# Performance work log

Hardware: AMD Instinct MI355X
Metric: run time of the kernel (lower is better)

## Reference

```python
import jax, jax.numpy as jnp
import numpy as np

BS, T, N, DIM = 16, 2048, 2048, 128

def setup_inputs() -> dict:
    key = jax.random.key(0)
    k1, k2, k3 = jax.random.split(key, 3)
    aud_feats = jax.random.normal(k1, (BS, T, DIM), dtype=jnp.float32)
    semantic_feats = jax.random.normal(k2, (BS, N, DIM), dtype=jnp.float32)
    W = jax.random.normal(k3, (1, 3 * DIM), dtype=jnp.float32) * 0.02
    b = jnp.zeros((1,), dtype=jnp.float32)
    return {"aud_feats": aud_feats, "semantic_feats": semantic_feats, "W": W, "b": b}


def reference(aud_feats, semantic_feats, W, b):
    # S[b,i,j] = Linear(cat(h_t, h_n, h_t*h_n)) decomposed into three rank-1 pieces
    dim = aud_feats.shape[-1]
    w1 = W[0, :dim]
    w2 = W[0, dim:2 * dim]
    w3 = W[0, 2 * dim:]
    S = (jnp.einsum('btd,d->bt', aud_feats, w1)[:, :, None]
         + jnp.einsum('bnd,d->bn', semantic_feats, w2)[:, None, :]
         + jnp.einsum('btd,bnd->btn', aud_feats * w3, semantic_feats)
         + b[0])  # [bs, t, n]
    at = jax.nn.softmax(S, axis=2)                     # attend over semantic tokens
    bw = jax.nn.softmax(jnp.max(S, axis=2), axis=1)    # [bs, t]
    h_con_a2 = jnp.einsum('bt,btd->bd', bw, aud_feats)[:, None, :]   # [bs,1,d], broadcasts
    h_con_w = jnp.einsum('btn,bnd->btd', at, semantic_feats)          # [bs,t,d]
    flow_matrix = jnp.concatenate(
        [aud_feats, h_con_w, aud_feats * h_con_w, aud_feats * h_con_a2], axis=2)
    return flow_matrix
```

## Files before the change

kernel.cpp:

```cpp
#include <hip/hip_runtime.h>
#include <stdint.h>

#define BSZ 16
#define TT  2048
#define NSEM 2048
#define DIM 128
#define ORS 1024
#define PSTR 68

typedef __attribute__((ext_vector_type(8))) short short8;
typedef __attribute__((ext_vector_type(4))) float floatx4;

__device__ __forceinline__ unsigned short f2bf(float f){
  unsigned u = __float_as_uint(f);
  return (unsigned short)((u + 0x7fffu + ((u >> 16) & 1u)) >> 16);
}
__device__ __forceinline__ void ld8f(const float* p, float* v){
  floatx4 a = *(const floatx4*)p;
  floatx4 b = *(const floatx4*)(p + 4);
  v[0]=a[0]; v[1]=a[1]; v[2]=a[2]; v[3]=a[3];
  v[4]=b[0]; v[5]=b[1]; v[6]=b[2]; v[7]=b[3];
}
__device__ __forceinline__ void gload_lds16(const unsigned short* g, unsigned short* l){
  __builtin_amdgcn_global_load_lds((const __attribute__((address_space(1))) void*)g,
                                   (__attribute__((address_space(3))) void*)l, 16, 0, 0);
}


__global__ __launch_bounds__(256) void prep_kernel(const float* __restrict__ sem,
                                                   const float* __restrict__ W,
                                                   float* __restrict__ colB,
                                                   unsigned short* __restrict__ outw){
  __shared__ unsigned short tile[DIM * 72];
  const int tid = threadIdx.x;
  const int b  = blockIdx.x >> 5;
  const int n0 = (blockIdx.x & 31) * 64;

  const int r = tid >> 2, cc = tid & 3, c = cc * 32;
  const float* src = sem + ((size_t)(b * NSEM + n0 + r)) * DIM + c;
  float v[32];
  ld8f(src, v); ld8f(src + 8, v + 8); ld8f(src + 16, v + 16); ld8f(src + 24, v + 24);
  alignas(16) unsigned short bf[32];
  float cpart = 0.f;
  #pragma unroll
  for (int j = 0; j < 32; ++j){
    bf[j] = f2bf(v[j]);
    cpart += v[j] * W[DIM + c + j];
  }
  {
    const int nblk = (n0 >> 4) + (r >> 4);
    const int l15r = r & 15;
    unsigned short* base = outw + ((size_t)(b * TT + nblk * 4 + cc)) * ORS + 512;
    const uint4* s4 = (const uint4*)bf;
    #pragma unroll
    for (int q = 0; q < 4; ++q)
      *(uint4*)(base + q * 128 + l15r * 8) = s4[q];
  }
  #pragma unroll
  for (int j = 0; j < 32; ++j) tile[(c + j) * 72 + r] = bf[j];
  cpart += __shfl_xor(cpart, 1);
  cpart += __shfl_xor(cpart, 2);
  if (cc == 0) colB[b * NSEM + n0 + r] = cpart;
  __syncthreads();

  {
    const int kt = tid >> 7, dc = (tid >> 4) & 7, l15 = tid & 15;
    const int d = dc * 16 + l15;
    const int ntile = n0 >> 6;
    unsigned short* base = outw + ((size_t)(b * TT + 512 + ntile * 16 + kt * 8 + dc)) * ORS + 512;
    #pragma unroll
    for (int q = 0; q < 4; ++q){
      uint4 tv = *(const uint4*)&tile[d * 72 + kt * 32 + q * 8];
      *(uint4*)(base + q * 128 + l15 * 8) = tv;
    }
  }
}

__global__ __launch_bounds__(256, 2) void flash_kernel(const float* __restrict__ aud,
                                                    const float* __restrict__ W,
                                                    const float* __restrict__ colB,
                                                    float* __restrict__ m_ws,
                                                    float* __restrict__ outf,
                                                    const unsigned short* __restrict__ outw){
  __shared__ alignas(16) unsigned short kvt[2][16][512];
  __shared__ alignas(16) unsigned short pbuf[4][16 * PSTR];

  const int tid  = threadIdx.x;
  const int wv   = tid >> 6;
  const int lane = tid & 63;
  const int quad = lane >> 4;
  const int l15  = lane & 15;
  const int b    = blockIdx.x >> 5;
  const int t0w  = (blockIdx.x & 31) * 64 + wv * 16;

  const unsigned short* stage = outw + (size_t)b * TT * ORS + 512 + lane * 8;

  #pragma unroll
  for (int jj = 0; jj < 4; ++jj){
    const int j = wv * 4 + jj;
    gload_lds16(stage + (size_t)j * ORS, &kvt[0][j][0]);
  }

  const float* audRow = aud + ((size_t)b * TT + t0w + l15) * DIM;
  short8 qf[4];
  float rowA_part = 0.f;
  #pragma unroll
  for (int kc = 0; kc < 4; ++kc){
    int d0 = kc * 32 + quad * 8;
    float av[8], w3v[8], w1v[8];
    ld8f(audRow + d0, av);
    ld8f(W + 2 * DIM + d0, w3v);
    ld8f(W + d0, w1v);
    alignas(16) unsigned short tmp[8];
    #pragma unroll
    for (int j = 0; j < 8; ++j){
      tmp[j] = f2bf(av[j] * w3v[j]);
      rowA_part += av[j] * w1v[j];
    }
    qf[kc] = *(const short8*)tmp;
  }
  rowA_part += __shfl_xor(rowA_part, 16);
  rowA_part += __shfl_xor(rowA_part, 32);

  float m_run = -1e30f, l_run = 0.f;
  float m_true = -1e30f;
  floatx4 o[8];
  #pragma unroll
  for (int dc = 0; dc < 8; ++dc){
    #pragma unroll
    for (int r = 0; r < 4; ++r) o[dc][r] = 0.f;
  }

  const float* colBb = colB + b * NSEM;
  unsigned short* pb = &pbuf[wv][0];

  __syncthreads();

  for (int it = 0; it < 32; ++it){
    const int n0 = it * 64;

    const int cV = 512 + it * 16;
    short8 vf[16];
    #pragma unroll
    for (int i = 0; i < 16; ++i) vf[i] = *(const short8*)(stage + (size_t)(cV + i) * ORS);

    if (it + 1 < 32){
      #pragma unroll
      for (int jj = 0; jj < 4; ++jj){
        const int j = wv * 4 + jj;
        gload_lds16(stage + (size_t)((it + 1) * 16 + j) * ORS, &kvt[(it + 1) & 1][j][0]);
      }
    }
    __builtin_amdgcn_sched_barrier(0);

    const unsigned short* kvb = &kvt[it & 1][0][0] + lane * 8;

    floatx4 cbv[4];
    #pragma unroll
    for (int s = 0; s < 4; ++s) cbv[s] = *(const floatx4*)(colBb + n0 + s*16 + quad*4);

    floatx4 sacc[4];
    #pragma unroll
    for (int s = 0; s < 4; ++s){ sacc[s][0]=0.f; sacc[s][1]=0.f; sacc[s][2]=0.f; sacc[s][3]=0.f; }
    #pragma unroll
    for (int s = 0; s < 4; ++s){
      #pragma unroll
      for (int kc = 0; kc < 4; ++kc){
        short8 kf = *(const short8*)(kvb + (s*4 + kc) * 512);
        sacc[s] = __builtin_amdgcn_mfma_f32_16x16x32_bf16(kf, qf[kc], sacc[s], 0, 0, 0);
      }
    }

    float v[4][4];
    #pragma unroll
    for (int s = 0; s < 4; ++s){
      #pragma unroll
      for (int r = 0; r < 4; ++r) v[s][r] = sacc[s][r] + cbv[s][r];
    }
    float mq[4];
    #pragma unroll
    for (int s = 0; s < 4; ++s)
      mq[s] = fmaxf(fmaxf(v[s][0], v[s][1]), fmaxf(v[s][2], v[s][3]));
    float mx = fmaxf(fmaxf(mq[0], mq[1]), fmaxf(mq[2], mq[3]));
    mx = fmaxf(mx, __shfl_xor(mx, 16));
    mx = fmaxf(mx, __shfl_xor(mx, 32));
    m_true = fmaxf(m_true, mx);

    const bool defer = (__all(mx - m_run <= 8.0f) != 0);
    float al = 1.0f;
    if (!defer){
      float mnew = fmaxf(m_run, mx);
      al = __expf(m_run - mnew);
      m_run = mnew;
    }
    float e[4][4];
    #pragma unroll
    for (int s = 0; s < 4; ++s){
      #pragma unroll
      for (int r = 0; r < 4; ++r) e[s][r] = __expf(v[s][r] - m_run);
    }
    float sq[4];
    #pragma unroll
    for (int s = 0; s < 4; ++s)
      sq[s] = (e[s][0] + e[s][1]) + (e[s][2] + e[s][3]);
    float ps = (sq[0] + sq[1]) + (sq[2] + sq[3]);
    ps += __shfl_xor(ps, 16);
    ps += __shfl_xor(ps, 32);
    l_run = l_run * al + ps;

    #pragma unroll
    for (int s = 0; s < 4; ++s){
      unsigned u0 = (unsigned)f2bf(e[s][0]) | ((unsigned)f2bf(e[s][1]) << 16);
      unsigned u1 = (unsigned)f2bf(e[s][2]) | ((unsigned)f2bf(e[s][3]) << 16);
      unsigned short* pr = pb + l15 * PSTR + s * 16 + quad * 4;
      *(unsigned*)(pr)     = u0;
      *(unsigned*)(pr + 2) = u1;
    }

    if (!defer){
      float aB[4];
      #pragma unroll
      for (int r = 0; r < 4; ++r) aB[r] = __shfl(al, quad*4 + r);
      #pragma unroll
      for (int dc = 0; dc < 8; ++dc){
        #pragma unroll
        for (int r = 0; r < 4; ++r) o[dc][r] *= aB[r];
      }
    }

    asm volatile("s_waitcnt lgkmcnt(0)" ::: "memory");
    short8 pf0 = *(const short8*)(pb + l15 * PSTR + quad * 8);
    short8 pf1 = *(const short8*)(pb + l15 * PSTR + 32 + quad * 8);

    #pragma unroll
    for (int kt = 0; kt < 2; ++kt){
      short8 pf = kt ? pf1 : pf0;
      #pragma unroll
      for (int dc = 0; dc < 8; ++dc)
        o[dc] = __builtin_amdgcn_mfma_f32_16x16x32_bf16(pf, vf[kt*8 + dc], o[dc], 0, 0, 0);
    }

    __syncthreads();
  }

  float rl = 1.0f / l_run;
  float rB[4];
  #pragma unroll
  for (int r = 0; r < 4; ++r) rB[r] = __shfl(rl, quad*4 + r);
  float* outB = outf + ((size_t)b * TT + t0w) * 512 + 128;
  #pragma unroll
  for (int dc = 0; dc < 8; ++dc){
    #pragma unroll
    for (int r = 0; r < 4; ++r)
      outB[(size_t)(quad*4 + r) * 512 + dc*16 + l15] = o[dc][r] * rB[r];
  }
  if (quad == 0)
    m_ws[(size_t)b * TT + t0w + l15] = m_true + rowA_part;
}

__global__ __launch_bounds__(256) void bw1_kernel(const float* __restrict__ m_ws,
                                                  float* __restrict__ pmax){
  __shared__ float sA[4];
  const int b = blockIdx.x >> 3, ch = blockIdx.x & 7, tid = threadIdx.x;
  float v = m_ws[(size_t)b * TT + ch * 256 + tid];
  #pragma unroll
  for (int off = 1; off < 64; off <<= 1) v = fmaxf(v, __shfl_xor(v, off));
  if ((tid & 63) == 0) sA[tid >> 6] = v;
  __syncthreads();
  if (tid == 0)
    pmax[blockIdx.x] = fmaxf(fmaxf(sA[0], sA[1]), fmaxf(sA[2], sA[3]));
}

__global__ __launch_bounds__(256) void bw2_kernel(const float* __restrict__ aud,
                                                  const float* __restrict__ m_ws,
                                                  const float* __restrict__ pmax,
                                                  float* __restrict__ gpart,
                                                  float* __restrict__ part){
  __shared__ float wbuf[256];
  __shared__ float red[16 * 128];
  __shared__ float gs4[4];
  const int b = blockIdx.x >> 3, ch = blockIdx.x & 7, tid = threadIdx.x;

  float gmax = pmax[b * 8];
  #pragma unroll
  for (int i = 1; i < 8; ++i) gmax = fmaxf(gmax, pmax[b * 8 + i]);

  float w = __expf(m_ws[(size_t)b * TT + ch * 256 + tid] - gmax);
  wbuf[tid] = w;
  float sm = w;
  #pragma unroll
  for (int off = 1; off < 64; off <<= 1) sm += __shfl_xor(sm, off);
  if ((tid & 63) == 0) gs4[tid >> 6] = sm;
  __syncthreads();
  if (tid == 0) gpart[blockIdx.x] = (gs4[0] + gs4[1]) + (gs4[2] + gs4[3]);

  const int dg = tid & 15, q = tid >> 4;
  float acc[8] = {0,0,0,0,0,0,0,0};
  const float* ab = aud + ((size_t)b * TT + ch * 256 + q * 16) * DIM + dg * 8;
  for (int i = 0; i < 16; ++i){
    float av[8];
    ld8f(ab + (size_t)i * DIM, av);
    float wt = wbuf[q * 16 + i];
    #pragma unroll
    for (int j = 0; j < 8; ++j) acc[j] += wt * av[j];
  }
  #pragma unroll
  for (int j = 0; j < 8; ++j) red[q * 128 + dg * 8 + j] = acc[j];
  __syncthreads();
  if (tid < 128){
    float s = 0.f;
    #pragma unroll
    for (int q2 = 0; q2 < 16; ++q2) s += red[q2 * 128 + tid];
    part[(size_t)blockIdx.x * 128 + tid] = s;
  }
}

__global__ __launch_bounds__(256) void epi_kernel(const float* __restrict__ aud,
                                                  const float* __restrict__ gpart,
                                                  const float* __restrict__ part,
                                                  float* __restrict__ out){
  __shared__ float a2s[DIM];
  int id = blockIdx.x * 256 + threadIdx.x;
  int c = id & 15;
  int t = (id >> 4) & (TT - 1);
  int b = id >> 15;
  size_t row = (size_t)b * TT + t;

  if (threadIdx.x < 128){
    const int d = threadIdx.x;
    float s = 0.f, g = 0.f;
    #pragma unroll
    for (int ch = 0; ch < 8; ++ch){
      s += part[(size_t)(b * 8 + ch) * 128 + d];
      g += gpart[b * 8 + ch];
    }
    a2s[d] = s / g;
  }
  __syncthreads();

  float av[8], gv[8], hv[8];
  ld8f(aud + row * DIM + c * 8, av);
  ld8f(out + row * 512 + 128 + c * 8, hv);
  #pragma unroll
  for (int j = 0; j < 8; ++j) gv[j] = a2s[c * 8 + j];

  floatx4 o0a, o0b, o2a, o2b, o3a, o3b;
  #pragma unroll
  for (int j = 0; j < 4; ++j){
    o0a[j] = av[j];           o0b[j] = av[4+j];
    o2a[j] = av[j]*hv[j];     o2b[j] = av[4+j]*hv[4+j];
    o3a[j] = av[j]*gv[j];     o3b[j] = av[4+j]*gv[4+j];
  }
  float* ob = out + row * 512 + c * 8;
  *(floatx4*)(ob)       = o0a;  *(floatx4*)(ob + 4)   = o0b;
  *(floatx4*)(ob + 256) = o2a;  *(floatx4*)(ob + 260) = o2b;
  *(floatx4*)(ob + 384) = o3a;  *(floatx4*)(ob + 388) = o3b;
}

extern "C" void kernel_launch(void* const* d_in, const int* in_sizes, int n_in,
                              void* d_out, int out_size, void* d_ws, size_t ws_size,
                              hipStream_t stream){
  const float* aud = (const float*)d_in[0];
  const float* sem = (const float*)d_in[1];
  const float* W   = (const float*)d_in[2];
  float* out = (float*)d_out;
  unsigned short* outw = (unsigned short*)d_out;

  float* ws    = (float*)d_ws;
  float* m_ws  = ws;
  float* colB  = m_ws + (size_t)BSZ * TT;
  float* a2_ws = colB + (size_t)BSZ * NSEM;
  float* pmax  = a2_ws + BSZ * DIM;
  float* gpart = pmax + 128;
  float* part  = gpart + 128;

  prep_kernel <<<512, 256, 0, stream>>>(sem, W, colB, outw);
  flash_kernel<<<512, 256, 0, stream>>>(aud, W, colB, m_ws, out, outw);
  bw1_kernel  <<<128, 256, 0, stream>>>(m_ws, pmax);
  bw2_kernel  <<<128, 256, 0, stream>>>(aud, m_ws, pmax, gpart, part);
  epi_kernel  <<<(BSZ * TT * 16) / 256, 256, 0, stream>>>(aud, gpart, part, out);
}
```

Before: 197.3 us.

## Split flash kernel over two KV halves per block with in-LDS merge, exp2 softmax

The flash kernel now runs 512 threads per block. Two wave groups each process half of the semantic tokens and keep separate online-softmax state, which is merged through LDS at the end. This doubles in-flight waves and halves the serial loop length per wave. Softmax switches to the base-2 domain: log2e is folded into q and colB, exp2 is used, and the final max is rescaled by ln2. The P buffer uses XOR swizzling with packed bf16 conversion to reduce LDS bank conflicts and conversion instructions. In exchange the kernel pays extra LDS use, a merge step and register pressure under launch_bounds(512,4).

Result: slower. 372.6 us (+88.9%).

```diff
diff --git a/kernel.cpp b/kernel.cpp
--- a/kernel.cpp
+++ b/kernel.cpp
@@ -6,7 +6,8 @@
 #define NSEM 2048
 #define DIM 128
 #define ORS 1024
-#define PSTR 68
+#define LOG2E 1.4426950408889634f
+#define LN2   0.6931471805599453f
 
 typedef __attribute__((ext_vector_type(8))) short short8;
 typedef __attribute__((ext_vector_type(4))) float floatx4;
@@ -14,6 +15,18 @@
 __device__ __forceinline__ unsigned short f2bf(float f){
   unsigned u = __float_as_uint(f);
   return (unsigned short)((u + 0x7fffu + ((u >> 16) & 1u)) >> 16);
+}
+__device__ __forceinline__ unsigned pkbf(float a, float b){
+  unsigned r;
+  asm("v_cvt_pk_bf16_f32 %0, %1, %2" : "=v"(r) : "v"(a), "v"(b));
+  return r;
+}
+__device__ __forceinline__ float e2(float x){
+#if __has_builtin(__builtin_amdgcn_exp2f)
+  return __builtin_amdgcn_exp2f(x);
+#else
+  return exp2f(x);
+#endif
 }
 __device__ __forceinline__ void ld8f(const float* p, float* v){
   floatx4 a = *(const floatx4*)p;
@@ -60,7 +73,7 @@
   for (int j = 0; j < 32; ++j) tile[(c + j) * 72 + r] = bf[j];
   cpart += __shfl_xor(cpart, 1);
   cpart += __shfl_xor(cpart, 2);
-  if (cc == 0) colB[b * NSEM + n0 + r] = cpart;
+  if (cc == 0) colB[b * NSEM + n0 + r] = cpart * LOG2E;
   __syncthreads();
 
   {
@@ -76,30 +89,30 @@
   }
 }
 
-__global__ __launch_bounds__(256, 2) void flash_kernel(const float* __restrict__ aud,
+__global__ __launch_bounds__(512, 4) void flash_kernel(const float* __restrict__ aud,
                                                     const float* __restrict__ W,
                                                     const float* __restrict__ colB,
                                                     float* __restrict__ m_ws,
                                                     float* __restrict__ outf,
                                                     const unsigned short* __restrict__ outw){
-  __shared__ alignas(16) unsigned short kvt[2][16][512];
-  __shared__ alignas(16) unsigned short pbuf[4][16 * PSTR];
+  __shared__ alignas(16) unsigned short kvt[2][2][16][512];
+  __shared__ alignas(16) unsigned short pbuf[8][1024];
 
   const int tid  = threadIdx.x;
   const int wv   = tid >> 6;
   const int lane = tid & 63;
   const int quad = lane >> 4;
   const int l15  = lane & 15;
+  const int h    = wv >> 2;
+  const int tg   = wv & 3;
   const int b    = blockIdx.x >> 5;
-  const int t0w  = (blockIdx.x & 31) * 64 + wv * 16;
+  const int t0w  = (blockIdx.x & 31) * 64 + tg * 16;
 
   const unsigned short* stage = outw + (size_t)b * TT * ORS + 512 + lane * 8;
 
   #pragma unroll
-  for (int jj = 0; jj < 4; ++jj){
-    const int j = wv * 4 + jj;
-    gload_lds16(stage + (size_t)j * ORS, &kvt[0][j][0]);
-  }
+  for (int jj = 0; jj < 4; ++jj)
+    gload_lds16(stage + (size_t)(h * 256 + tg * 4 + jj) * ORS, &kvt[h][0][tg * 4 + jj][0]);
 
   const float* audRow = aud + ((size_t)b * TT + t0w + l15) * DIM;
   short8 qf[4];
@@ -114,7 +127,7 @@
     alignas(16) unsigned short tmp[8];
     #pragma unroll
     for (int j = 0; j < 8; ++j){
-      tmp[j] = f2bf(av[j] * w3v[j]);
+      tmp[j] = f2bf(av[j] * (w3v[j] * LOG2E));
       rowA_part += av[j] * w1v[j];
     }
     qf[kc] = *(const short8*)tmp;
@@ -133,31 +146,31 @@
 
   const float* colBb = colB + b * NSEM;
   unsigned short* pb = &pbuf[wv][0];
-
-  __syncthreads();
-
-  for (int it = 0; it < 32; ++it){
-    const int n0 = it * 64;
-
-    const int cV = 512 + it * 16;
+  const int swz = (l15 & 7);
+
+  __syncthreads();
+
+  for (int it = 0; it < 16; ++it){
+    const int n0 = h * 1024 + it * 64;
+
+    floatx4 cbv[4];
+    #pragma unroll
+    for (int s = 0; s < 4; ++s) cbv[s] = *(const floatx4*)(colBb + n0 + s*16 + quad*4);
+
+    if (it + 1 < 16){
+      #pragma unroll
+      for (int jj = 0; jj < 4; ++jj)
+        gload_lds16(stage + (size_t)(h * 256 + (it + 1) * 16 + tg * 4 + jj) * ORS,
+                    &kvt[h][(it + 1) & 1][tg * 4 + jj][0]);
+    }
+
+    const int cV = 512 + (h * 16 + it) * 16;
     short8 vf[16];
     #pragma unroll
     for (int i = 0; i < 16; ++i) vf[i] = *(const short8*)(stage + (size_t)(cV + i) * ORS);
-
-    if (it + 1 < 32){
-      #pragma unroll
-      for (int jj = 0; jj < 4; ++jj){
-        const int j = wv * 4 + jj;
-        gload_lds16(stage + (size_t)((it + 1) * 16 + j) * ORS, &kvt[(it + 1) & 1][j][0]);
-      }
-    }
     __builtin_amdgcn_sched_barrier(0);
 
-    const unsigned short* kvb = &kvt[it & 1][0][0] + lane * 8;
-
-    floatx4 cbv[4];
-    #pragma unroll
-    for (int s = 0; s < 4; ++s) cbv[s] = *(const floatx4*)(colBb + n0 + s*16 + quad*4);
+    const unsigned short* kvb = &kvt[h][it & 1][0][0] + lane * 8;
 
     floatx4 sacc[4];
     #pragma unroll
@@ -190,14 +203,14 @@
     float al = 1.0f;
     if (!defer){
       float mnew = fmaxf(m_run, mx);
-      al = __expf(m_run - mnew);
+      al = e2(m_run - mnew);
       m_run = mnew;
     }
     float e[4][4];
     #pragma unroll
     for (int s = 0; s < 4; ++s){
       #pragma unroll
-      for (int r = 0; r < 4; ++r) e[s][r] = __expf(v[s][r] - m_run);
+      for (int r = 0; r < 4; ++r) e[s][r] = e2(v[s][r] - m_run);
     }
     float sq[4];
     #pragma unroll
@@ -210,11 +223,11 @@
 
     #pragma unroll
     for (int s = 0; s < 4; ++s){
-      unsigned u0 = (unsigned)f2bf(e[s][0]) | ((unsigned)f2bf(e[s][1]) << 16);
-      unsigned u1 = (unsigned)f2bf(e[s][2]) | ((unsigned)f2bf(e[s][3]) << 16);
-      unsigned short* pr = pb + l15 * PSTR + s * 16 + quad * 4;
-      *(unsigned*)(pr)     = u0;
-      *(unsigned*)(pr + 2) = u1;
+      unsigned u0 = pkbf(e[s][0], e[s][1]);
+      unsigned u1 = pkbf(e[s][2], e[s][3]);
+      const int chk = 2*s + (quad >> 1);
+      unsigned short* pr = pb + l15 * 64 + ((chk ^ swz) << 3) + (quad & 1) * 4;
+      *(uint64_t*)pr = (uint64_t)u0 | ((uint64_t)u1 << 32);
     }
 
     if (!defer){
@@ -229,8 +242,8 @@
     }
 
     asm volatile("s_waitcnt lgkmcnt(0)" ::: "memory");
-    short8 pf0 = *(const short8*)(pb + l15 * PSTR + quad * 8);
-    short8 pf1 = *(const short8*)(pb + l15 * PSTR + 32 + quad * 8);
+    short8 pf0 = *(const short8*)(pb + l15 * 64 + ((quad       ^ swz) << 3));
+    short8 pf1 = *(const short8*)(pb + l15 * 64 + (((4 | quad) ^ swz) << 3));
 
     #pragma unroll
     for (int kt = 0; kt < 2; ++kt){
@@ -243,19 +256,48 @@
     __syncthreads();
   }
 
-  float rl = 1.0f / l_run;
-  float rB[4];
-  #pragma unroll
-  for (int r = 0; r < 4; ++r) rB[r] = __shfl(rl, quad*4 + r);
-  float* outB = outf + ((size_t)b * TT + t0w) * 512 + 128;
-  #pragma unroll
-  for (int dc = 0; dc < 8; ++dc){
-    #pragma unroll
-    for (int r = 0; r < 4; ++r)
-      outB[(size_t)(quad*4 + r) * 512 + dc*16 + l15] = o[dc][r] * rB[r];
-  }
-  if (quad == 0)
-    m_ws[(size_t)b * TT + t0w + l15] = m_true + rowA_part;
+  float* Ob  = (float*)(&kvt[0][0][0][0]);
+  float* mlp = Ob + 4 * 16 * 128;
+  if (h == 1){
+    #pragma unroll
+    for (int dc = 0; dc < 8; ++dc){
+      #pragma unroll
+      for (int r = 0; r < 4; ++r)
+        Ob[(tg * 16 + quad * 4 + r) * 128 + dc * 16 + l15] = o[dc][r];
+    }
+    if (quad == 0){
+      mlp[tg * 48 +      l15] = m_run;
+      mlp[tg * 48 + 16 + l15] = l_run;
+      mlp[tg * 48 + 32 + l15] = m_true;
+    }
+  }
+  __syncthreads();
+  if (h == 0){
+    float mp  = mlp[tg * 48 +      l15];
+    float lp  = mlp[tg * 48 + 16 + l15];
+    float mtp = mlp[tg * 48 + 32 + l15];
+    float M  = fmaxf(m_run, mp);
+    float sA = e2(m_run - M);
+    float sB = e2(mp - M);
+    float lm = l_run * sA + lp * sB;
+    float mt = fmaxf(m_true, mtp);
+    float rl = 1.0f / lm;
+    float fa = sA * rl, fb = sB * rl;
+    float fA[4], fB[4];
+    #pragma unroll
+    for (int r = 0; r < 4; ++r){ fA[r] = __shfl(fa, quad*4 + r); fB[r] = __shfl(fb, quad*4 + r); }
+    float* outB = outf + ((size_t)b * TT + t0w) * 512 + 128;
+    #pragma unroll
+    for (int dc = 0; dc < 8; ++dc){
+      #pragma unroll
+      for (int r = 0; r < 4; ++r){
+        float op = Ob[(tg * 16 + quad * 4 + r) * 128 + dc * 16 + l15];
+        outB[(size_t)(quad*4 + r) * 512 + dc*16 + l15] = o[dc][r] * fA[r] + op * fB[r];
+      }
+    }
+    if (quad == 0)
+      m_ws[(size_t)b * TT + t0w + l15] = mt * LN2 + rowA_part;
+  }
 }
 
 __global__ __launch_bounds__(256) void bw1_kernel(const float* __restrict__ m_ws,
@@ -375,7 +417,7 @@
   float* part  = gpart + 128;
 
   prep_kernel <<<512, 256, 0, stream>>>(sem, W, colB, outw);
-  flash_kernel<<<512, 256, 0, stream>>>(aud, W, colB, m_ws, out, outw);
+  flash_kernel<<<512, 512, 0, stream>>>(aud, W, colB, m_ws, out, outw);
   bw1_kernel  <<<128, 256, 0, stream>>>(m_ws, pmax);
   bw2_kernel  <<<128, 256, 0, stream>>>(aud, m_ws, pmax, gpart, part);
   epi_kernel  <<<(BSZ * TT * 16) / 256, 256, 0, stream>>>(aud, gpart, part, out);
```

## Split attention over key halves with merge kernel and base-2 exponentials

Applied to the files above, without the earlier changes.

The flash kernel now splits the semantic-token dimension into two halves, doubling the block count to 1024. Each half writes unnormalized partial outputs and running max/sum statistics into spare regions of the output buffer, and a new merge kernel combines them with a log-sum-exp rescale. Scores are pre-scaled by log2(e) so the kernel can use exp2 in place of exp, and bf16 packing uses the hardware pack-convert instruction. The aim is more parallelism and occupancy on the GPU. The cost is an extra kernel launch and extra global traffic for the partial results.

Measured after the change: 215.0 us. 1.09x slower.

```diff
diff --git a/kernel.cpp b/kernel.cpp
--- a/kernel.cpp
+++ b/kernel.cpp
@@ -7,6 +7,8 @@
 #define DIM 128
 #define ORS 1024
 #define PSTR 68
+#define LOG2E 1.4426950408889634f
+#define LN2   0.6931471805599453f
 
 typedef __attribute__((ext_vector_type(8))) short short8;
 typedef __attribute__((ext_vector_type(4))) float floatx4;
@@ -14,6 +16,18 @@
 __device__ __forceinline__ unsigned short f2bf(float f){
   unsigned u = __float_as_uint(f);
   return (unsigned short)((u + 0x7fffu + ((u >> 16) & 1u)) >> 16);
+}
+__device__ __forceinline__ unsigned pkbf(float a, float b){
+  unsigned r;
+  asm("v_cvt_pk_bf16_f32 %0, %1, %2" : "=v"(r) : "v"(a), "v"(b));
+  return r;
+}
+__device__ __forceinline__ float e2(float x){
+#if __has_builtin(__builtin_amdgcn_exp2f)
+  return __builtin_amdgcn_exp2f(x);
+#else
+  return exp2f(x);
+#endif
 }
 __device__ __forceinline__ void ld8f(const float* p, float* v){
   floatx4 a = *(const floatx4*)p;
@@ -60,7 +74,7 @@
   for (int j = 0; j < 32; ++j) tile[(c + j) * 72 + r] = bf[j];
   cpart += __shfl_xor(cpart, 1);
   cpart += __shfl_xor(cpart, 2);
-  if (cc == 0) colB[b * NSEM + n0 + r] = cpart;
+  if (cc == 0) colB[b * NSEM + n0 + r] = cpart * LOG2E;
   __syncthreads();
 
   {
@@ -79,7 +93,6 @@
 __global__ __launch_bounds__(256, 2) void flash_kernel(const float* __restrict__ aud,
                                                     const float* __restrict__ W,
                                                     const float* __restrict__ colB,
-                                                    float* __restrict__ m_ws,
                                                     float* __restrict__ outf,
                                                     const unsigned short* __restrict__ outw){
   __shared__ alignas(16) unsigned short kvt[2][16][512];
@@ -90,15 +103,18 @@
   const int lane = tid & 63;
   const int quad = lane >> 4;
   const int l15  = lane & 15;
-  const int b    = blockIdx.x >> 5;
-  const int t0w  = (blockIdx.x & 31) * 64 + wv * 16;
+  const int b    = blockIdx.x >> 6;
+  const int sub  = blockIdx.x & 63;
+  const int tb   = sub >> 1;
+  const int h    = sub & 1;
+  const int t0w  = tb * 64 + wv * 16;
 
   const unsigned short* stage = outw + (size_t)b * TT * ORS + 512 + lane * 8;
 
   #pragma unroll
   for (int jj = 0; jj < 4; ++jj){
     const int j = wv * 4 + jj;
-    gload_lds16(stage + (size_t)j * ORS, &kvt[0][j][0]);
+    gload_lds16(stage + (size_t)(h * 256 + j) * ORS, &kvt[0][j][0]);
   }
 
   const float* audRow = aud + ((size_t)b * TT + t0w + l15) * DIM;
@@ -114,7 +130,7 @@
     alignas(16) unsigned short tmp[8];
     #pragma unroll
     for (int j = 0; j < 8; ++j){
-      tmp[j] = f2bf(av[j] * w3v[j]);
+      tmp[j] = f2bf(av[j] * (w3v[j] * LOG2E));
       rowA_part += av[j] * w1v[j];
     }
     qf[kc] = *(const short8*)tmp;
@@ -136,19 +152,21 @@
 
   __syncthreads();
 
-  for (int it = 0; it < 32; ++it){
-    const int n0 = it * 64;
-
-    const int cV = 512 + it * 16;
+  for (int it = 0; it < 16; ++it){
+    const int nt = h * 16 + it;
+    const int n0 = nt * 64;
+
+    const int cV = 512 + nt * 16;
     short8 vf[16];
     #pragma unroll
     for (int i = 0; i < 16; ++i) vf[i] = *(const short8*)(stage + (size_t)(cV + i) * ORS);
 
-    if (it + 1 < 32){
+    if (it + 1 < 16){
       #pragma unroll
       for (int jj = 0; jj < 4; ++jj){
         const int j = wv * 4 + jj;
-        gload_lds16(stage + (size_t)((it + 1) * 16 + j) * ORS, &kvt[(it + 1) & 1][j][0]);
+        gload_lds16(stage + (size_t)(h * 256 + (it + 1) * 16 + j) * ORS,
+                    &kvt[(it + 1) & 1][j][0]);
       }
     }
     __builtin_amdgcn_sched_barrier(0);
@@ -190,14 +208,14 @@
     float al = 1.0f;
     if (!defer){
       float mnew = fmaxf(m_run, mx);
-      al = __expf(m_run - mnew);
+      al = e2(m_run - mnew);
       m_run = mnew;
     }
     float e[4][4];
     #pragma unroll
     for (int s = 0; s < 4; ++s){
       #pragma unroll
-      for (int r = 0; r < 4; ++r) e[s][r] = __expf(v[s][r] - m_run);
+      for (int r = 0; r < 4; ++r) e[s][r] = e2(v[s][r] - m_run);
     }
     float sq[4];
     #pragma unroll
@@ -210,8 +228,8 @@
 
     #pragma unroll
     for (int s = 0; s < 4; ++s){
-      unsigned u0 = (unsigned)f2bf(e[s][0]) | ((unsigned)f2bf(e[s][1]) << 16);
-      unsigned u1 = (unsigned)f2bf(e[s][2]) | ((unsigned)f2bf(e[s][3]) << 16);
+      unsigned u0 = pkbf(e[s][0], e[s][1]);
+      unsigned u1 = pkbf(e[s][2], e[s][3]);
       unsigned short* pr = pb + l15 * PSTR + s * 16 + quad * 4;
       *(unsigned*)(pr)     = u0;
       *(unsigned*)(pr + 2) = u1;
@@ -243,19 +261,64 @@
     __syncthreads();
   }
 
-  float rl = 1.0f / l_run;
-  float rB[4];
-  #pragma unroll
-  for (int r = 0; r < 4; ++r) rB[r] = __shfl(rl, quad*4 + r);
-  float* outB = outf + ((size_t)b * TT + t0w) * 512 + 128;
-  #pragma unroll
-  for (int dc = 0; dc < 8; ++dc){
-    #pragma unroll
-    for (int r = 0; r < 4; ++r)
-      outB[(size_t)(quad*4 + r) * 512 + dc*16 + l15] = o[dc][r] * rB[r];
-  }
-  if (quad == 0)
-    m_ws[(size_t)b * TT + t0w + l15] = m_true + rowA_part;
+  if (h == 0){
+    float* outB = outf + ((size_t)b * TT + t0w) * 512 + 128;
+    #pragma unroll
+    for (int dc = 0; dc < 8; ++dc){
+      #pragma unroll
+      for (int r = 0; r < 4; ++r)
+        outB[(size_t)(quad*4 + r) * 512 + dc*16 + l15] = o[dc][r];
+    }
+  } else {
+    float* outB = outf + ((size_t)(b * TT + 1024 + (t0w >> 1))) * 512 + 256;
+    #pragma unroll
+    for (int dc = 0; dc < 8; ++dc){
+      #pragma unroll
+      for (int r = 0; r < 4; ++r)
+        outB[(size_t)(quad*2 + (r >> 1)) * 512 + (r & 1) * 128 + dc*16 + l15] = o[dc][r];
+    }
+  }
+  if (quad == 0){
+    float* mlp = outf + ((size_t)(b * TT + 1024 + ((t0w + l15) >> 1))) * 512
+               + (l15 & 1) * 8 + h * 4;
+    mlp[0] = m_run;
+    mlp[1] = l_run;
+    mlp[2] = m_true * LN2 + rowA_part;
+  }
+}
+
+__global__ __launch_bounds__(256) void merge_kernel(float* __restrict__ out,
+                                                    float* __restrict__ m_ws){
+  int id = blockIdx.x * 256 + threadIdx.x;
+  int c = id & 15;
+  int t = (id >> 4) & (TT - 1);
+  int b = id >> 15;
+  size_t row  = (size_t)b * TT + t;
+  size_t mrow = (size_t)b * TT + 1024 + (t >> 1);
+  int mo = t & 1;
+
+  float O0[8], O1[8];
+  ld8f(out + row * 512 + 128 + c * 8, O0);
+  ld8f(out + mrow * 512 + 256 + mo * 128 + c * 8, O1);
+  const float* mlp = out + mrow * 512 + mo * 8;
+  float m0 = mlp[0], l0 = mlp[1], mt0 = mlp[2];
+  float m1 = mlp[4], l1 = mlp[5], mt1 = mlp[6];
+
+  float M  = fmaxf(m0, m1);
+  float fA = e2(m0 - M), fB = e2(m1 - M);
+  float rl = 1.0f / (l0 * fA + l1 * fB);
+  fA *= rl; fB *= rl;
+
+  floatx4 h0, h1;
+  #pragma unroll
+  for (int j = 0; j < 4; ++j){
+    h0[j] = O0[j]   * fA + O1[j]   * fB;
+    h1[j] = O0[4+j] * fA + O1[4+j] * fB;
+  }
+  float* dst = out + row * 512 + 128 + c * 8;
+  *(floatx4*)(dst)     = h0;
+  *(floatx4*)(dst + 4) = h1;
+  if (c == 0) m_ws[row] = fmaxf(mt0, mt1);
 }
 
 __global__ __launch_bounds__(256) void bw1_kernel(const float* __restrict__ m_ws,
@@ -375,7 +438,8 @@
   float* part  = gpart + 128;
 
   prep_kernel <<<512, 256, 0, stream>>>(sem, W, colB, outw);
-  flash_kernel<<<512, 256, 0, stream>>>(aud, W, colB, m_ws, out, outw);
+  flash_kernel<<<1024, 256, 0, stream>>>(aud, W, colB, out, outw);
+  merge_kernel<<<2048, 256, 0, stream>>>(out, m_ws);
   bw1_kernel  <<<128, 256, 0, stream>>>(m_ws, pmax);
   bw2_kernel  <<<128, 256, 0, stream>>>(aud, m_ws, pmax, gpart, part);
   epi_kernel  <<<(BSZ * TT * 16) / 256, 256, 0, stream>>>(aud, gpart, part, out);
```
